# Kernel tuning notes

Hardware: AMD Instinct MI355X
Metric: run time of the kernel (lower is better)

Reference implementation:

```python
import jax, jax.numpy as jnp
import numpy as np

B, S, F, D, VOCAB, H = 1024, 512, 4, 32, 100001, 64
LN_EPS = 1e-3  # keras LayerNormalization default


def setup_inputs() -> dict:
    key = jax.random.key(0)
    ks = jax.random.split(key, 16)
    sd = 0.05
    return {
        "values": jax.random.normal(ks[0], (B, S, F), jnp.float32),
        "names": jax.random.randint(ks[1], (B, S), 0, VOCAB),
        "emb_table": jax.random.normal(ks[2], (VOCAB, D), jnp.float32) * sd,
        "W_num": jax.random.normal(ks[3], (F, D), jnp.float32) * sd,
        "b_num": jnp.zeros((D,), jnp.float32),
        "Wq": jax.random.normal(ks[4], (D, D), jnp.float32) * sd,
        "bq": jnp.zeros((D,), jnp.float32),
        "Wv": jax.random.normal(ks[5], (D, D), jnp.float32) * sd,
        "bv": jnp.zeros((D,), jnp.float32),
        "attn_scale": jnp.ones((D,), jnp.float32),
        "Wp": jax.random.normal(ks[6], (D, H), jnp.float32) * sd,
        "bp": jnp.zeros((H,), jnp.float32),
        "ln_gamma": jnp.ones((H,), jnp.float32),
        "ln_beta": jnp.zeros((H,), jnp.float32),
        "Ws": jax.random.normal(ks[7], (H, 2), jnp.float32) * sd,
    }


def reference(values, names, emb_table, W_num, b_num, Wq, bq, Wv, bv,
              attn_scale, Wp, bp, ln_gamma, ln_beta, Ws):
    # embeddings + numerical projection  [B,S,D]
    v = values @ W_num + b_num
    e = emb_table[names]
    mix = e + v
    # query from last position, value/key from the rest
    q = mix[:, -1:, :] @ Wq + bq          # [B,1,D]
    val = mix[:, :-1, :] @ Wv + bv        # [B,S-1,D]
    # keras AdditiveAttention (use_scale=True): score = sum(scale*tanh(q+k))
    scores = jnp.sum(attn_scale * jnp.tanh(q[:, :, None, :] + val[:, None, :, :]), axis=-1)  # [B,1,S-1]
    attn = jax.nn.softmax(scores, axis=-1)
    emb_out = jnp.einsum('bij,bjd->bid', attn, val)  # [B,1,D]
    # broadcast add then mean over sequence
    context = jnp.mean(emb_out + mix, axis=1)        # [B,D]
    # predictor: Dense(relu) + LayerNorm(axis=1 == features)
    h = jax.nn.relu(context @ Wp + bp)               # [B,H]
    mu = jnp.mean(h, axis=1, keepdims=True)
    var = jnp.var(h, axis=1, keepdims=True)
    h = (h - mu) * jax.lax.rsqrt(var + LN_EPS) * ln_gamma + ln_beta
    # scorer: Dense(2, softmax, no bias)
    score = jax.nn.softmax(h @ Ws, axis=-1)          # [B,2]
    return (score, emb_out, attn, h)
```

## Files before the change

kernel.cpp:

```cpp
#include <hip/hip_runtime.h>
#include <math.h>

constexpr int Bsz   = 1024;
constexpr int S     = 512;
constexpr int SV    = 511;
constexpr int D     = 32;
constexpr int F     = 4;
constexpr int H     = 64;
constexpr int BDIM  = 256;
constexpr int VOCAB = 100001;

__device__ __forceinline__ float fast_tanh(float x) {
  const float ex = __expf(2.f * x);
  return 1.f - 2.f * __builtin_amdgcn_rcpf(ex + 1.f);
}

__global__ __launch_bounds__(BDIM) void build_table(
    const float* __restrict__ emb, const float* __restrict__ Wv,
    float* __restrict__ T, int vocab)
{
  __shared__ float sWv[D * D];
  for (int i = threadIdx.x; i < D * D; i += BDIM) sWv[i] = Wv[i];
  __syncthreads();
  const int lr  = threadIdx.x >> 5;
  const int k   = threadIdx.x & 31;
  const int row = blockIdx.x * 8 + lr;
  if (row < vocab) {
    const float4* e4 = reinterpret_cast<const float4*>(emb + (size_t)row * D);
    float acc = 0.f;
    #pragma unroll
    for (int c = 0; c < 8; c++) {
      const float4 v = e4[c];
      acc += v.x * sWv[(4 * c + 0) * D + k] + v.y * sWv[(4 * c + 1) * D + k]
           + v.z * sWv[(4 * c + 2) * D + k] + v.w * sWv[(4 * c + 3) * D + k];
    }
    T[(size_t)row * 64 + k]      = emb[(size_t)row * D + k];
    T[(size_t)row * 64 + 32 + k] = acc;
  }
}

__global__ __launch_bounds__(BDIM) void attn_fused_tab(
    const float* __restrict__ values, const int* __restrict__ names,
    const float* __restrict__ T,
    const float* __restrict__ W_num, const float* __restrict__ b_num,
    const float* __restrict__ Wq,    const float* __restrict__ bq,
    const float* __restrict__ Wv,    const float* __restrict__ bv,
    const float* __restrict__ attn_scale,
    const float* __restrict__ Wp,    const float* __restrict__ bp,
    const float* __restrict__ ln_g,  const float* __restrict__ ln_b,
    const float* __restrict__ Ws,
    float* __restrict__ out_score, float* __restrict__ out_emb,
    float* __restrict__ out_attn,  float* __restrict__ out_h)
{
  __shared__ float sWnum[F * D];
  __shared__ float sbnum[D];
  __shared__ float sWq[D * D];
  __shared__ float sWv[D * D];
  __shared__ float sbv[D];
  __shared__ float sscale[D];
  __shared__ float sW2[F * D];
  __shared__ float sbias2[D];
  __shared__ float sq[D];
  __shared__ float smixq[D];
  __shared__ float sred[4][72];
  __shared__ float sredS[4];
  __shared__ float sML[2];
  __shared__ float sctx[D];
  __shared__ float sWp[D * H];

  const int b    = blockIdx.x;
  const int tid  = threadIdx.x;
  const int lane = tid & 63;
  const int wv   = tid >> 6;

  for (int i = tid; i < F * D; i += BDIM) sWnum[i] = W_num[i];
  if (tid < D) { sbnum[tid] = b_num[tid]; sbv[tid] = bv[tid]; sscale[tid] = attn_scale[tid]; }
  for (int i = tid; i < D * D; i += BDIM) { sWq[i] = Wq[i]; sWv[i] = Wv[i]; }
  for (int i = tid; i < D * H; i += BDIM) sWp[i] = Wp[i];
  __syncthreads();

  if (tid < F * D) {
    const int f = tid >> 5, k = tid & 31;
    float a = 0.f;
    #pragma unroll
    for (int m = 0; m < D; m++) a += sWnum[f * D + m] * sWv[m * D + k];
    sW2[f * D + k] = a;
  }
  if (tid >= F * D && tid < F * D + D) {
    const int k = tid - F * D;
    float a = sbv[k];
    #pragma unroll
    for (int m = 0; m < D; m++) a += sbnum[m] * sWv[m * D + k];
    sbias2[k] = a;
  }
  __syncthreads();

  if (tid < D) {
    const int    name = names[b * S + (S - 1)];
    const float* vr   = values + (size_t)(b * S + (S - 1)) * F;
    smixq[tid] = T[(size_t)name * 64 + tid] + sbnum[tid]
               + vr[0] * sWnum[tid] + vr[1] * sWnum[D + tid]
               + vr[2] * sWnum[2 * D + tid] + vr[3] * sWnum[3 * D + tid];
  }
  __syncthreads();
  if (tid < D) {
    float a = bq[tid];
    #pragma unroll
    for (int k = 0; k < D; k++) a += smixq[k] * sWq[k * D + tid];
    sq[tid] = a;
  }
  __syncthreads();

  float esum[D], acc[D];
  #pragma unroll
  for (int k = 0; k < D; k++) { esum[k] = 0.f; acc[k] = 0.f; }
  float vsum[F] = {0.f, 0.f, 0.f, 0.f};
  float mloc = -INFINITY, lloc = 0.f;
  float sc0 = 0.f, sc1 = 0.f;
  const bool has2 = (tid < SV - BDIM);

  auto row = [&](int j, float& sout) {
    const int    name = names[b * S + j];
    const float4 v4   = *reinterpret_cast<const float4*>(values + (size_t)(b * S + j) * F);
    const float4* t4  = reinterpret_cast<const float4*>(T + (size_t)name * 64);
    float val[D];
    #pragma unroll
    for (int c = 0; c < 8; c++) {
      const float4 ev = t4[c];
      esum[4 * c] += ev.x; esum[4 * c + 1] += ev.y; esum[4 * c + 2] += ev.z; esum[4 * c + 3] += ev.w;
      const float4 wvv = t4[8 + c];
      val[4 * c] = wvv.x; val[4 * c + 1] = wvv.y; val[4 * c + 2] = wvv.z; val[4 * c + 3] = wvv.w;
    }
    vsum[0] += v4.x; vsum[1] += v4.y; vsum[2] += v4.z; vsum[3] += v4.w;
    float s = 0.f;
    #pragma unroll
    for (int k = 0; k < D; k++) {
      val[k] += sbias2[k] + v4.x * sW2[k] + v4.y * sW2[D + k]
              + v4.z * sW2[2 * D + k] + v4.w * sW2[3 * D + k];
      s += sscale[k] * fast_tanh(sq[k] + val[k]);
    }
    sout = s;
    float w;
    if (s > mloc) {
      const float sf = __expf(mloc - s);
      lloc *= sf;
      #pragma unroll
      for (int k = 0; k < D; k++) acc[k] *= sf;
      mloc = s; w = 1.f;
    } else {
      w = __expf(s - mloc);
    }
    lloc += w;
    #pragma unroll
    for (int k = 0; k < D; k++) acc[k] += w * val[k];
  };

  row(tid, sc0);
  if (has2) row(tid + BDIM, sc1);

  float mw = mloc;
  #pragma unroll
  for (int off = 32; off; off >>= 1) mw = fmaxf(mw, __shfl_xor(mw, off));
  if (lane == 0) sredS[wv] = mw;
  __syncthreads();
  if (tid == 0) sML[0] = fmaxf(fmaxf(sredS[0], sredS[1]), fmaxf(sredS[2], sredS[3]));
  __syncthreads();
  const float M = sML[0];

  {
    const float adj = __expf(mloc - M);
    lloc *= adj;
    #pragma unroll
    for (int k = 0; k < D; k++) acc[k] *= adj;
  }

  float lw = lloc;
  #pragma unroll
  for (int off = 32; off; off >>= 1) lw += __shfl_xor(lw, off);
  #pragma unroll
  for (int f = 0; f < F; f++) {
    float vs = vsum[f];
    #pragma unroll
    for (int off = 32; off; off >>= 1) vs += __shfl_xor(vs, off);
    if (lane == 0) sred[wv][65 + f] = vs;
  }
  if (lane == 0) sred[wv][64] = lw;
  #pragma unroll
  for (int k = 0; k < D; k++) {
    float a = acc[k], e = esum[k];
    #pragma unroll
    for (int off = 32; off; off >>= 1) { a += __shfl_xor(a, off); e += __shfl_xor(e, off); }
    if (lane == 0) { sred[wv][k] = a; sred[wv][D + k] = e; }
  }
  __syncthreads();
  if (tid == 0) sML[1] = sred[0][64] + sred[1][64] + sred[2][64] + sred[3][64];
  __syncthreads();
  const float L    = sML[1];
  const float invL = 1.f / L;

  out_attn[(size_t)b * SV + tid] = __expf(sc0 - M) * invL;
  if (has2) out_attn[(size_t)b * SV + tid + BDIM] = __expf(sc1 - M) * invL;

  if (tid < D) {
    const float a  = sred[0][tid] + sred[1][tid] + sred[2][tid] + sred[3][tid];
    const float e  = sred[0][D + tid] + sred[1][D + tid] + sred[2][D + tid] + sred[3][D + tid];
    float vs[F];
    #pragma unroll
    for (int f = 0; f < F; f++) vs[f] = sred[0][65 + f] + sred[1][65 + f] + sred[2][65 + f] + sred[3][65 + f];
    const float vproj = vs[0] * sWnum[tid] + vs[1] * sWnum[D + tid]
                      + vs[2] * sWnum[2 * D + tid] + vs[3] * sWnum[3 * D + tid];
    const float mixsum = e + vproj + (float)SV * sbnum[tid];
    const float eo = a * invL;
    out_emb[(size_t)b * D + tid] = eo;
    sctx[tid] = eo + (mixsum + smixq[tid]) * (1.f / (float)S);
  }
  __syncthreads();

  if (tid < H) {
    float hv = bp[tid];
    #pragma unroll
    for (int d = 0; d < D; d++) hv += sctx[d] * sWp[d * H + tid];
    hv = fmaxf(hv, 0.f);
    float mu = hv;
    #pragma unroll
    for (int off = 32; off; off >>= 1) mu += __shfl_xor(mu, off);
    mu *= (1.f / 64.f);
    const float dv = hv - mu;
    float vv = dv * dv;
    #pragma unroll
    for (int off = 32; off; off >>= 1) vv += __shfl_xor(vv, off);
    vv *= (1.f / 64.f);
    const float hn = dv * rsqrtf(vv + 1e-3f) * ln_g[tid] + ln_b[tid];
    out_h[(size_t)b * H + tid] = hn;
    float s0 = hn * Ws[2 * tid], s1 = hn * Ws[2 * tid + 1];
    #pragma unroll
    for (int off = 32; off; off >>= 1) { s0 += __shfl_xor(s0, off); s1 += __shfl_xor(s1, off); }
    if (tid == 0) {
      const float mx = fmaxf(s0, s1);
      const float e0 = __expf(s0 - mx), e1 = __expf(s1 - mx);
      const float inv = 1.f / (e0 + e1);
      out_score[(size_t)b * 2]     = e0 * inv;
      out_score[(size_t)b * 2 + 1] = e1 * inv;
    }
  }
}

__global__ __launch_bounds__(BDIM) void attn_fused_gemv(
    const float* __restrict__ values, const int* __restrict__ names,
    const float* __restrict__ emb,
    const float* __restrict__ W_num, const float* __restrict__ b_num,
    const float* __restrict__ Wq,    const float* __restrict__ bq,
    const float* __restrict__ Wv,    const float* __restrict__ bv,
    const float* __restrict__ attn_scale,
    const float* __restrict__ Wp,    const float* __restrict__ bp,
    const float* __restrict__ ln_g,  const float* __restrict__ ln_b,
    const float* __restrict__ Ws,
    float* __restrict__ out_score, float* __restrict__ out_emb,
    float* __restrict__ out_attn,  float* __restrict__ out_h)
{
  __shared__ float sWnum[F * D];
  __shared__ float sbnum[D];
  __shared__ float sWq[D * D];
  __shared__ float sWv[D * D];
  __shared__ float sbv[D];
  __shared__ float sscale[D];
  __shared__ float sq[D];
  __shared__ float smixq[D];
  __shared__ float sred[4][2 * D];
  __shared__ float sredS[4];
  __shared__ float sML[2];
  __shared__ float sctx[D];
  __shared__ float sWp[D * H];

  const int b    = blockIdx.x;
  const int tid  = threadIdx.x;
  const int lane = tid & 63;
  const int wv   = tid >> 6;

  for (int i = tid; i < F * D; i += BDIM) sWnum[i] = W_num[i];
  if (tid < D) { sbnum[tid] = b_num[tid]; sbv[tid] = bv[tid]; sscale[tid] = attn_scale[tid]; }
  for (int i = tid; i < D * D; i += BDIM) { sWq[i] = Wq[i]; sWv[i] = Wv[i]; }
  for (int i = tid; i < D * H; i += BDIM) sWp[i] = Wp[i];
  __syncthreads();

  if (tid < D) {
    const int    name = names[b * S + (S - 1)];
    const float* vr   = values + (size_t)(b * S + (S - 1)) * F;
    smixq[tid] = emb[(size_t)name * D + tid] + sbnum[tid]
               + vr[0] * sWnum[tid] + vr[1] * sWnum[D + tid]
               + vr[2] * sWnum[2 * D + tid] + vr[3] * sWnum[3 * D + tid];
  }
  __syncthreads();
  if (tid < D) {
    float a = bq[tid];
    #pragma unroll
    for (int k = 0; k < D; k++) a += smixq[k] * sWq[k * D + tid];
    sq[tid] = a;
  }
  __syncthreads();

  float msum[D], acc[D];
  #pragma unroll
  for (int k = 0; k < D; k++) { msum[k] = 0.f; acc[k] = 0.f; }
  float mloc = -INFINITY, lloc = 0.f;
  float sc0 = 0.f, sc1 = 0.f;
  const bool has2 = (tid < SV - BDIM);

  auto row = [&](int j, float& sout) {
    const int    name = names[b * S + j];
    const float4 v4   = *reinterpret_cast<const float4*>(values + (size_t)(b * S + j) * F);
    const float4* e4p = reinterpret_cast<const float4*>(emb + (size_t)name * D);
    float mix[D];
    #pragma unroll
    for (int c = 0; c < 8; c++) {
      const float4 e = e4p[c];
      mix[4 * c] = e.x; mix[4 * c + 1] = e.y; mix[4 * c + 2] = e.z; mix[4 * c + 3] = e.w;
    }
    #pragma unroll
    for (int k = 0; k < D; k++) {
      mix[k] += sbnum[k] + v4.x * sWnum[k] + v4.y * sWnum[D + k]
              + v4.z * sWnum[2 * D + k] + v4.w * sWnum[3 * D + k];
      msum[k] += mix[k];
    }
    float val[D];
    #pragma unroll
    for (int k = 0; k < D; k++) val[k] = sbv[k];
    for (int m = 0; m < D; m++) {
      const float mv = mix[m];
      #pragma unroll
      for (int k = 0; k < D; k++) val[k] += mv * sWv[m * D + k];
    }
    float s = 0.f;
    #pragma unroll
    for (int k = 0; k < D; k++) s += sscale[k] * fast_tanh(sq[k] + val[k]);
    sout = s;
    float w;
    if (s > mloc) {
      const float sf = __expf(mloc - s);
      lloc *= sf;
      #pragma unroll
      for (int k = 0; k < D; k++) acc[k] *= sf;
      mloc = s; w = 1.f;
    } else {
      w = __expf(s - mloc);
    }
    lloc += w;
    #pragma unroll
    for (int k = 0; k < D; k++) acc[k] += w * val[k];
  };

  row(tid, sc0);
  if (has2) row(tid + BDIM, sc1);

  float mw = mloc;
  #pragma unroll
  for (int off = 32; off; off >>= 1) mw = fmaxf(mw, __shfl_xor(mw, off));
  if (lane == 0) sredS[wv] = mw;
  __syncthreads();
  if (tid == 0) sML[0] = fmaxf(fmaxf(sredS[0], sredS[1]), fmaxf(sredS[2], sredS[3]));
  __syncthreads();
  const float M = sML[0];
  {
    const float adj = __expf(mloc - M);
    lloc *= adj;
    #pragma unroll
    for (int k = 0; k < D; k++) acc[k] *= adj;
  }
  float lw = lloc;
  #pragma unroll
  for (int off = 32; off; off >>= 1) lw += __shfl_xor(lw, off);
  if (lane == 0) sredS[wv] = lw;
  #pragma unroll
  for (int k = 0; k < D; k++) {
    float a = acc[k], mm = msum[k];
    #pragma unroll
    for (int off = 32; off; off >>= 1) { a += __shfl_xor(a, off); mm += __shfl_xor(mm, off); }
    if (lane == 0) { sred[wv][k] = a; sred[wv][D + k] = mm; }
  }
  __syncthreads();
  if (tid == 0) sML[1] = sredS[0] + sredS[1] + sredS[2] + sredS[3];
  __syncthreads();
  const float L    = sML[1];
  const float invL = 1.f / L;

  out_attn[(size_t)b * SV + tid] = __expf(sc0 - M) * invL;
  if (has2) out_attn[(size_t)b * SV + tid + BDIM] = __expf(sc1 - M) * invL;

  if (tid < D) {
    const float a  = sred[0][tid] + sred[1][tid] + sred[2][tid] + sred[3][tid];
    const float mm = sred[0][D + tid] + sred[1][D + tid] + sred[2][D + tid] + sred[3][D + tid];
    const float eo = a * invL;
    out_emb[(size_t)b * D + tid] = eo;
    sctx[tid] = eo + (mm + smixq[tid]) * (1.f / (float)S);
  }
  __syncthreads();

  if (tid < H) {
    float hv = bp[tid];
    #pragma unroll
    for (int d = 0; d < D; d++) hv += sctx[d] * sWp[d * H + tid];
    hv = fmaxf(hv, 0.f);
    float mu = hv;
    #pragma unroll
    for (int off = 32; off; off >>= 1) mu += __shfl_xor(mu, off);
    mu *= (1.f / 64.f);
    const float dv = hv - mu;
    float vv = dv * dv;
    #pragma unroll
    for (int off = 32; off; off >>= 1) vv += __shfl_xor(vv, off);
    vv *= (1.f / 64.f);
    const float hn = dv * rsqrtf(vv + 1e-3f) * ln_g[tid] + ln_b[tid];
    out_h[(size_t)b * H + tid] = hn;
    float s0 = hn * Ws[2 * tid], s1 = hn * Ws[2 * tid + 1];
    #pragma unroll
    for (int off = 32; off; off >>= 1) { s0 += __shfl_xor(s0, off); s1 += __shfl_xor(s1, off); }
    if (tid == 0) {
      const float mx = fmaxf(s0, s1);
      const float e0 = __expf(s0 - mx), e1 = __expf(s1 - mx);
      const float inv = 1.f / (e0 + e1);
      out_score[(size_t)b * 2]     = e0 * inv;
      out_score[(size_t)b * 2 + 1] = e1 * inv;
    }
  }
}

extern "C" void kernel_launch(void* const* d_in, const int* in_sizes, int n_in,
                              void* d_out, int out_size, void* d_ws, size_t ws_size,
                              hipStream_t stream) {
  const float* values = (const float*)d_in[0];
  const int*   names  = (const int*)d_in[1];
  const float* emb    = (const float*)d_in[2];
  const float* W_num  = (const float*)d_in[3];
  const float* b_num  = (const float*)d_in[4];
  const float* Wq     = (const float*)d_in[5];
  const float* bq     = (const float*)d_in[6];
  const float* Wv     = (const float*)d_in[7];
  const float* bv     = (const float*)d_in[8];
  const float* scal   = (const float*)d_in[9];
  const float* Wp     = (const float*)d_in[10];
  const float* bp     = (const float*)d_in[11];
  const float* ln_g   = (const float*)d_in[12];
  const float* ln_b   = (const float*)d_in[13];
  const float* Ws     = (const float*)d_in[14];

  float* out      = (float*)d_out;
  float* o_score  = out;
  float* o_emb    = o_score + (size_t)Bsz * 2;
  float* o_attn   = o_emb   + (size_t)Bsz * D;
  float* o_h      = o_attn  + (size_t)Bsz * SV;

  const size_t tab_bytes = (size_t)VOCAB * 64 * sizeof(float);
  if (ws_size >= tab_bytes) {
    float* T = (float*)d_ws;
    hipLaunchKernelGGL(build_table, dim3((VOCAB + 7) / 8), dim3(BDIM), 0, stream, emb, Wv, T, VOCAB);
    hipLaunchKernelGGL(attn_fused_tab, dim3(Bsz), dim3(BDIM), 0, stream,
                       values, names, T, W_num, b_num, Wq, bq, Wv, bv, scal,
                       Wp, bp, ln_g, ln_b, Ws, o_score, o_emb, o_attn, o_h);
  } else {
    hipLaunchKernelGGL(attn_fused_gemv, dim3(Bsz), dim3(BDIM), 0, stream,
                       values, names, emb, W_num, b_num, Wq, bq, Wv, bv, scal,
                       Wp, bp, ln_g, ln_b, Ws, o_score, o_emb, o_attn, o_h);
  }
}
```

Measured before the change: 161.6 us.

## Store precomputed emb/value table in bf16 and drop online-softmax max tracking

Result: slower. 177.2 us (+9.7%).

```diff
diff --git a/kernel.cpp b/kernel.cpp
--- a/kernel.cpp
+++ b/kernel.cpp
@@ -1,4 +1,5 @@
 #include <hip/hip_runtime.h>
+#include <hip/hip_bf16.h>
 #include <math.h>
 
 constexpr int Bsz   = 1024;
@@ -9,42 +10,70 @@
 constexpr int H     = 64;
 constexpr int BDIM  = 256;
 constexpr int VOCAB = 100001;
+constexpr size_t TAB_BYTES = (size_t)VOCAB * 64 * 2;
 
 __device__ __forceinline__ float fast_tanh(float x) {
   const float ex = __expf(2.f * x);
   return 1.f - 2.f * __builtin_amdgcn_rcpf(ex + 1.f);
 }
 
-__global__ __launch_bounds__(BDIM) void build_table(
+__device__ __forceinline__ void unpack8(uint4 u, float* f) {
+  f[0] = __uint_as_float(u.x << 16); f[1] = __uint_as_float(u.x & 0xffff0000u);
+  f[2] = __uint_as_float(u.y << 16); f[3] = __uint_as_float(u.y & 0xffff0000u);
+  f[4] = __uint_as_float(u.z << 16); f[5] = __uint_as_float(u.z & 0xffff0000u);
+  f[6] = __uint_as_float(u.w << 16); f[7] = __uint_as_float(u.w & 0xffff0000u);
+}
+
+__global__ __launch_bounds__(BDIM) void build_tab(
     const float* __restrict__ emb, const float* __restrict__ Wv,
-    float* __restrict__ T, int vocab)
+    const float* __restrict__ W_num, const float* __restrict__ b_num,
+    const float* __restrict__ bv,
+    __hip_bfloat16* __restrict__ T, float* __restrict__ wsc)
 {
   __shared__ float sWv[D * D];
   for (int i = threadIdx.x; i < D * D; i += BDIM) sWv[i] = Wv[i];
   __syncthreads();
-  const int lr  = threadIdx.x >> 5;
-  const int k   = threadIdx.x & 31;
+
+  if (blockIdx.x == gridDim.x - 1) {
+    const int tid = threadIdx.x;
+    if (tid < F * D) {
+      const int f = tid >> 5, k = tid & 31;
+      float a = 0.f;
+      #pragma unroll
+      for (int m = 0; m < D; m++) a += W_num[f * D + m] * sWv[m * D + k];
+      wsc[k * 4 + f] = a;
+    } else if (tid < F * D + D) {
+      const int k = tid - F * D;
+      float a = bv[k];
+      #pragma unroll
+      for (int m = 0; m < D; m++) a += b_num[m] * sWv[m * D + k];
+      wsc[F * D + k] = a;
+    }
+    return;
+  }
+
+  const int lr = threadIdx.x >> 5, k = threadIdx.x & 31;
   const int row = blockIdx.x * 8 + lr;
-  if (row < vocab) {
+  if (row < VOCAB) {
     const float4* e4 = reinterpret_cast<const float4*>(emb + (size_t)row * D);
-    float acc = 0.f;
+    float a = 0.f;
     #pragma unroll
     for (int c = 0; c < 8; c++) {
       const float4 v = e4[c];
-      acc += v.x * sWv[(4 * c + 0) * D + k] + v.y * sWv[(4 * c + 1) * D + k]
-           + v.z * sWv[(4 * c + 2) * D + k] + v.w * sWv[(4 * c + 3) * D + k];
-    }
-    T[(size_t)row * 64 + k]      = emb[(size_t)row * D + k];
-    T[(size_t)row * 64 + 32 + k] = acc;
-  }
-}
-
-__global__ __launch_bounds__(BDIM) void attn_fused_tab(
+      a += v.x * sWv[(4 * c + 0) * D + k] + v.y * sWv[(4 * c + 1) * D + k]
+         + v.z * sWv[(4 * c + 2) * D + k] + v.w * sWv[(4 * c + 3) * D + k];
+    }
+    T[(size_t)row * 64 + k]      = __float2bfloat16(emb[(size_t)row * D + k]);
+    T[(size_t)row * 64 + 32 + k] = __float2bfloat16(a);
+  }
+}
+
+__global__ __launch_bounds__(BDIM) void attn_main(
     const float* __restrict__ values, const int* __restrict__ names,
-    const float* __restrict__ T,
+    const __hip_bfloat16* __restrict__ T, const float* __restrict__ wsc,
+    const float* __restrict__ emb,
     const float* __restrict__ W_num, const float* __restrict__ b_num,
     const float* __restrict__ Wq,    const float* __restrict__ bq,
-    const float* __restrict__ Wv,    const float* __restrict__ bv,
     const float* __restrict__ attn_scale,
     const float* __restrict__ Wp,    const float* __restrict__ bp,
     const float* __restrict__ ln_g,  const float* __restrict__ ln_b,
@@ -52,139 +81,89 @@
     float* __restrict__ out_score, float* __restrict__ out_emb,
     float* __restrict__ out_attn,  float* __restrict__ out_h)
 {
-  __shared__ float sWnum[F * D];
-  __shared__ float sbnum[D];
-  __shared__ float sWq[D * D];
-  __shared__ float sWv[D * D];
-  __shared__ float sbv[D];
-  __shared__ float sscale[D];
-  __shared__ float sW2[F * D];
-  __shared__ float sbias2[D];
-  __shared__ float sq[D];
+  __shared__ float sW2T[D][4];
+  __shared__ float sQS[D][2];
   __shared__ float smixq[D];
-  __shared__ float sred[4][72];
-  __shared__ float sredS[4];
-  __shared__ float sML[2];
+  __shared__ float sred[4][69];
   __shared__ float sctx[D];
-  __shared__ float sWp[D * H];
-
-  const int b    = blockIdx.x;
-  const int tid  = threadIdx.x;
-  const int lane = tid & 63;
-  const int wv   = tid >> 6;
-
-  for (int i = tid; i < F * D; i += BDIM) sWnum[i] = W_num[i];
-  if (tid < D) { sbnum[tid] = b_num[tid]; sbv[tid] = bv[tid]; sscale[tid] = attn_scale[tid]; }
-  for (int i = tid; i < D * D; i += BDIM) { sWq[i] = Wq[i]; sWv[i] = Wv[i]; }
-  for (int i = tid; i < D * H; i += BDIM) sWp[i] = Wp[i];
-  __syncthreads();
-
-  if (tid < F * D) {
-    const int f = tid >> 5, k = tid & 31;
-    float a = 0.f;
-    #pragma unroll
-    for (int m = 0; m < D; m++) a += sWnum[f * D + m] * sWv[m * D + k];
-    sW2[f * D + k] = a;
-  }
-  if (tid >= F * D && tid < F * D + D) {
-    const int k = tid - F * D;
-    float a = sbv[k];
-    #pragma unroll
-    for (int m = 0; m < D; m++) a += sbnum[m] * sWv[m * D + k];
-    sbias2[k] = a;
-  }
-  __syncthreads();
-
-  if (tid < D) {
-    const int    name = names[b * S + (S - 1)];
-    const float* vr   = values + (size_t)(b * S + (S - 1)) * F;
-    smixq[tid] = T[(size_t)name * 64 + tid] + sbnum[tid]
-               + vr[0] * sWnum[tid] + vr[1] * sWnum[D + tid]
-               + vr[2] * sWnum[2 * D + tid] + vr[3] * sWnum[3 * D + tid];
+  __shared__ float sL[1];
+
+  const int b = blockIdx.x, tid = threadIdx.x, lane = tid & 63, wv = tid >> 6;
+
+  if (tid < 128) sW2T[tid >> 2][tid & 3] = wsc[tid];
+  if (tid < D) {
+    const int    nq = names[b * S + (S - 1)];
+    const float* vr = values + (size_t)(b * S + (S - 1)) * F;
+    smixq[tid] = emb[(size_t)nq * D + tid] + b_num[tid]
+               + vr[0] * W_num[tid] + vr[1] * W_num[D + tid]
+               + vr[2] * W_num[2 * D + tid] + vr[3] * W_num[3 * D + tid];
   }
   __syncthreads();
   if (tid < D) {
     float a = bq[tid];
     #pragma unroll
-    for (int k = 0; k < D; k++) a += smixq[k] * sWq[k * D + tid];
-    sq[tid] = a;
-  }
-  __syncthreads();
+    for (int m = 0; m < D; m++) a += smixq[m] * Wq[m * D + tid];
+    sQS[tid][0] = a + wsc[128 + tid];
+    sQS[tid][1] = attn_scale[tid];
+  }
+  __syncthreads();
+
+  const int  j0 = tid, j1 = tid + BDIM;
+  const bool has1 = (j1 < SV);
+  const int  n0 = names[b * S + j0];
+  const int  n1 = names[b * S + (has1 ? j1 : j0)];
+  float4 v0 = *reinterpret_cast<const float4*>(values + (size_t)(b * S + j0) * F);
+  float4 v1 = *reinterpret_cast<const float4*>(values + (size_t)(b * S + (has1 ? j1 : j0)) * F);
+  const uint4* g0 = reinterpret_cast<const uint4*>(T + (size_t)n0 * 64);
+  const uint4* g1 = reinterpret_cast<const uint4*>(T + (size_t)n1 * 64);
+  uint4 E00 = g0[0], E01 = g0[1], E02 = g0[2], E03 = g0[3];
+  uint4 W00 = g0[4], W01 = g0[5], W02 = g0[6], W03 = g0[7];
+  uint4 E10 = g1[0], E11 = g1[1], E12 = g1[2], E13 = g1[3];
+  uint4 W10 = g1[4], W11 = g1[5], W12 = g1[6], W13 = g1[7];
 
   float esum[D], acc[D];
   #pragma unroll
   for (int k = 0; k < D; k++) { esum[k] = 0.f; acc[k] = 0.f; }
-  float vsum[F] = {0.f, 0.f, 0.f, 0.f};
-  float mloc = -INFINITY, lloc = 0.f;
-  float sc0 = 0.f, sc1 = 0.f;
-  const bool has2 = (tid < SV - BDIM);
-
-  auto row = [&](int j, float& sout) {
-    const int    name = names[b * S + j];
-    const float4 v4   = *reinterpret_cast<const float4*>(values + (size_t)(b * S + j) * F);
-    const float4* t4  = reinterpret_cast<const float4*>(T + (size_t)name * 64);
-    float val[D];
-    #pragma unroll
-    for (int c = 0; c < 8; c++) {
-      const float4 ev = t4[c];
-      esum[4 * c] += ev.x; esum[4 * c + 1] += ev.y; esum[4 * c + 2] += ev.z; esum[4 * c + 3] += ev.w;
-      const float4 wvv = t4[8 + c];
-      val[4 * c] = wvv.x; val[4 * c + 1] = wvv.y; val[4 * c + 2] = wvv.z; val[4 * c + 3] = wvv.w;
-    }
-    vsum[0] += v4.x; vsum[1] += v4.y; vsum[2] += v4.z; vsum[3] += v4.w;
+  float lloc = 0.f, e0 = 0.f, e1 = 0.f;
+  float vs0 = v0.x, vs1 = v0.y, vs2 = v0.z, vs3 = v0.w;
+  if (has1) { vs0 += v1.x; vs1 += v1.y; vs2 += v1.z; vs3 += v1.w; }
+
+  auto dorow = [&](uint4 Ea, uint4 Eb, uint4 Ec, uint4 Ed,
+                   uint4 Wa, uint4 Wb, uint4 Wc, uint4 Wd, float4 vv) -> float {
+    float em[D], w[D], t[D];
+    unpack8(Ea, em); unpack8(Eb, em + 8); unpack8(Ec, em + 16); unpack8(Ed, em + 24);
+    unpack8(Wa, w);  unpack8(Wb, w + 8);  unpack8(Wc, w + 16);  unpack8(Wd, w + 24);
     float s = 0.f;
     #pragma unroll
     for (int k = 0; k < D; k++) {
-      val[k] += sbias2[k] + v4.x * sW2[k] + v4.y * sW2[D + k]
-              + v4.z * sW2[2 * D + k] + v4.w * sW2[3 * D + k];
-      s += sscale[k] * fast_tanh(sq[k] + val[k]);
-    }
-    sout = s;
-    float w;
-    if (s > mloc) {
-      const float sf = __expf(mloc - s);
-      lloc *= sf;
-      #pragma unroll
-      for (int k = 0; k < D; k++) acc[k] *= sf;
-      mloc = s; w = 1.f;
-    } else {
-      w = __expf(s - mloc);
-    }
-    lloc += w;
-    #pragma unroll
-    for (int k = 0; k < D; k++) acc[k] += w * val[k];
+      esum[k] += em[k];
+      const float tk = w[k] + sQS[k][0]
+                     + vv.x * sW2T[k][0] + vv.y * sW2T[k][1]
+                     + vv.z * sW2T[k][2] + vv.w * sW2T[k][3];
+      t[k] = tk;
+      s += sQS[k][1] * fast_tanh(tk);
+    }
+    const float e = __expf(s);
+    lloc += e;
+    #pragma unroll
+    for (int k = 0; k < D; k++) acc[k] = fmaf(e, t[k], acc[k]);
+    return e;
   };
 
-  row(tid, sc0);
-  if (has2) row(tid + BDIM, sc1);
-
-  float mw = mloc;
-  #pragma unroll
-  for (int off = 32; off; off >>= 1) mw = fmaxf(mw, __shfl_xor(mw, off));
-  if (lane == 0) sredS[wv] = mw;
-  __syncthreads();
-  if (tid == 0) sML[0] = fmaxf(fmaxf(sredS[0], sredS[1]), fmaxf(sredS[2], sredS[3]));
-  __syncthreads();
-  const float M = sML[0];
-
-  {
-    const float adj = __expf(mloc - M);
-    lloc *= adj;
-    #pragma unroll
-    for (int k = 0; k < D; k++) acc[k] *= adj;
-  }
-
-  float lw = lloc;
-  #pragma unroll
-  for (int off = 32; off; off >>= 1) lw += __shfl_xor(lw, off);
-  #pragma unroll
-  for (int f = 0; f < F; f++) {
-    float vs = vsum[f];
-    #pragma unroll
-    for (int off = 32; off; off >>= 1) vs += __shfl_xor(vs, off);
-    if (lane == 0) sred[wv][65 + f] = vs;
-  }
-  if (lane == 0) sred[wv][64] = lw;
+  e0 = dorow(E00, E01, E02, E03, W00, W01, W02, W03, v0);
+  if (has1) e1 = dorow(E10, E11, E12, E13, W10, W11, W12, W13, v1);
+
+  #pragma unroll
+  for (int off = 32; off; off >>= 1) lloc += __shfl_xor(lloc, off);
+  float v4s[4] = {vs0, vs1, vs2, vs3};
+  #pragma unroll
+  for (int f = 0; f < 4; f++) {
+    float x = v4s[f];
+    #pragma unroll
+    for (int off = 32; off; off >>= 1) x += __shfl_xor(x, off);
+    if (lane == 0) sred[wv][65 + f] = x;
+  }
+  if (lane == 0) sred[wv][64] = lloc;
   #pragma unroll
   for (int k = 0; k < D; k++) {
     float a = acc[k], e = esum[k];
@@ -193,54 +172,54 @@
     if (lane == 0) { sred[wv][k] = a; sred[wv][D + k] = e; }
   }
   __syncthreads();
-  if (tid == 0) sML[1] = sred[0][64] + sred[1][64] + sred[2][64] + sred[3][64];
-  __syncthreads();
-  const float L    = sML[1];
-  const float invL = 1.f / L;
-
-  out_attn[(size_t)b * SV + tid] = __expf(sc0 - M) * invL;
-  if (has2) out_attn[(size_t)b * SV + tid + BDIM] = __expf(sc1 - M) * invL;
-
-  if (tid < D) {
-    const float a  = sred[0][tid] + sred[1][tid] + sred[2][tid] + sred[3][tid];
-    const float e  = sred[0][D + tid] + sred[1][D + tid] + sred[2][D + tid] + sred[3][D + tid];
-    float vs[F];
-    #pragma unroll
-    for (int f = 0; f < F; f++) vs[f] = sred[0][65 + f] + sred[1][65 + f] + sred[2][65 + f] + sred[3][65 + f];
-    const float vproj = vs[0] * sWnum[tid] + vs[1] * sWnum[D + tid]
-                      + vs[2] * sWnum[2 * D + tid] + vs[3] * sWnum[3 * D + tid];
-    const float mixsum = e + vproj + (float)SV * sbnum[tid];
-    const float eo = a * invL;
+  if (tid == 0) sL[0] = sred[0][64] + sred[1][64] + sred[2][64] + sred[3][64];
+  __syncthreads();
+  const float invL = 1.f / sL[0];
+
+  out_attn[(size_t)b * SV + j0] = e0 * invL;
+  if (has1) out_attn[(size_t)b * SV + j1] = e1 * invL;
+
+  if (tid < D) {
+    const float aS = sred[0][tid] + sred[1][tid] + sred[2][tid] + sred[3][tid];
+    const float eS = sred[0][D + tid] + sred[1][D + tid] + sred[2][D + tid] + sred[3][D + tid];
+    float vp = 0.f;
+    #pragma unroll
+    for (int f = 0; f < 4; f++) {
+      const float vf = sred[0][65 + f] + sred[1][65 + f] + sred[2][65 + f] + sred[3][65 + f];
+      vp += vf * W_num[f * D + tid];
+    }
+    const float q  = sQS[tid][0] - wsc[128 + tid];
+    const float eo = aS * invL - q;
     out_emb[(size_t)b * D + tid] = eo;
-    sctx[tid] = eo + (mixsum + smixq[tid]) * (1.f / (float)S);
+    sctx[tid] = eo + (eS + vp + (float)SV * b_num[tid] + smixq[tid]) * (1.f / (float)S);
   }
   __syncthreads();
 
   if (tid < H) {
     float hv = bp[tid];
     #pragma unroll
-    for (int d = 0; d < D; d++) hv += sctx[d] * sWp[d * H + tid];
+    for (int d = 0; d < D; d++) hv += sctx[d] * Wp[d * H + tid];
     hv = fmaxf(hv, 0.f);
     float mu = hv;
     #pragma unroll
     for (int off = 32; off; off >>= 1) mu += __shfl_xor(mu, off);
     mu *= (1.f / 64.f);
     const float dv = hv - mu;
-    float vv = dv * dv;
-    #pragma unroll
-    for (int off = 32; off; off >>= 1) vv += __shfl_xor(vv, off);
-    vv *= (1.f / 64.f);
-    const float hn = dv * rsqrtf(vv + 1e-3f) * ln_g[tid] + ln_b[tid];
+    float vvv = dv * dv;
+    #pragma unroll
+    for (int off = 32; off; off >>= 1) vvv += __shfl_xor(vvv, off);
+    vvv *= (1.f / 64.f);
+    const float hn = dv * rsqrtf(vvv + 1e-3f) * ln_g[tid] + ln_b[tid];
     out_h[(size_t)b * H + tid] = hn;
     float s0 = hn * Ws[2 * tid], s1 = hn * Ws[2 * tid + 1];
     #pragma unroll
     for (int off = 32; off; off >>= 1) { s0 += __shfl_xor(s0, off); s1 += __shfl_xor(s1, off); }
     if (tid == 0) {
       const float mx = fmaxf(s0, s1);
-      const float e0 = __expf(s0 - mx), e1 = __expf(s1 - mx);
-      const float inv = 1.f / (e0 + e1);
-      out_score[(size_t)b * 2]     = e0 * inv;
-      out_score[(size_t)b * 2 + 1] = e1 * inv;
+      const float a0 = __expf(s0 - mx), a1 = __expf(s1 - mx);
+      const float inv = 1.f / (a0 + a1);
+      out_score[(size_t)b * 2]     = a0 * inv;
+      out_score[(size_t)b * 2 + 1] = a1 * inv;
     }
   }
 }
@@ -272,10 +251,7 @@
   __shared__ float sctx[D];
   __shared__ float sWp[D * H];
 
-  const int b    = blockIdx.x;
-  const int tid  = threadIdx.x;
-  const int lane = tid & 63;
-  const int wv   = tid >> 6;
+  const int b = blockIdx.x, tid = threadIdx.x, lane = tid & 63, wv = tid >> 6;
 
   for (int i = tid; i < F * D; i += BDIM) sWnum[i] = W_num[i];
   if (tid < D) { sbnum[tid] = b_num[tid]; sbv[tid] = bv[tid]; sscale[tid] = attn_scale[tid]; }
@@ -380,8 +356,7 @@
   __syncthreads();
   if (tid == 0) sML[1] = sredS[0] + sredS[1] + sredS[2] + sredS[3];
   __syncthreads();
-  const float L    = sML[1];
-  const float invL = 1.f / L;
+  const float L = sML[1], invL = 1.f / L;
 
   out_attn[(size_t)b * SV + tid] = __expf(sc0 - M) * invL;
   if (has2) out_attn[(size_t)b * SV + tid + BDIM] = __expf(sc1 - M) * invL;
@@ -416,10 +391,10 @@
     for (int off = 32; off; off >>= 1) { s0 += __shfl_xor(s0, off); s1 += __shfl_xor(s1, off); }
     if (tid == 0) {
       const float mx = fmaxf(s0, s1);
-      const float e0 = __expf(s0 - mx), e1 = __expf(s1 - mx);
-      const float inv = 1.f / (e0 + e1);
-      out_score[(size_t)b * 2]     = e0 * inv;
-      out_score[(size_t)b * 2 + 1] = e1 * inv;
+      const float a0 = __expf(s0 - mx), a1 = __expf(s1 - mx);
+      const float inv = 1.f / (a0 + a1);
+      out_score[(size_t)b * 2]     = a0 * inv;
+      out_score[(size_t)b * 2 + 1] = a1 * inv;
     }
   }
 }
@@ -449,12 +424,14 @@
   float* o_attn   = o_emb   + (size_t)Bsz * D;
   float* o_h      = o_attn  + (size_t)Bsz * SV;
 
-  const size_t tab_bytes = (size_t)VOCAB * 64 * sizeof(float);
-  if (ws_size >= tab_bytes) {
-    float* T = (float*)d_ws;
-    hipLaunchKernelGGL(build_table, dim3((VOCAB + 7) / 8), dim3(BDIM), 0, stream, emb, Wv, T, VOCAB);
-    hipLaunchKernelGGL(attn_fused_tab, dim3(Bsz), dim3(BDIM), 0, stream,
-                       values, names, T, W_num, b_num, Wq, bq, Wv, bv, scal,
+  const size_t need = TAB_BYTES + 256 * sizeof(float);
+  if (ws_size >= need) {
+    __hip_bfloat16* T = (__hip_bfloat16*)d_ws;
+    float* wsc = (float*)((char*)d_ws + TAB_BYTES);
+    hipLaunchKernelGGL(build_tab, dim3((VOCAB + 7) / 8 + 1), dim3(BDIM), 0, stream,
+                       emb, Wv, W_num, b_num, bv, T, wsc);
+    hipLaunchKernelGGL(attn_main, dim3(Bsz), dim3(BDIM), 0, stream,
+                       values, names, T, wsc, emb, W_num, b_num, Wq, bq, scal,
                        Wp, bp, ln_g, ln_b, Ws, o_score, o_emb, o_attn, o_h);
   } else {
     hipLaunchKernelGGL(attn_fused_gemv, dim3(Bsz), dim3(BDIM), 0, stream,
```
